# Performance work log

Hardware: AMD Instinct MI355X
Metric: run time of the kernel (lower is better)

Reference implementation:

```python
import jax, jax.numpy as jnp
import numpy as np

B, T, D = 2, 2048, 2048
N, K, H = 16, 8, 128  # num_heads, num_kv_heads, head_dim
SOFTCAP = 50.0
ROPE_BASE = 10000.0


def apply_rope(x, positions):
    # x: [B, L, heads, H], positions: [B, L]
    head_dim = x.shape[-1]
    fraction = 2.0 * jnp.arange(head_dim // 2, dtype=jnp.float32) / head_dim
    timescale = ROPE_BASE ** fraction  # [H/2]
    sinusoid = positions.astype(jnp.float32)[..., None] / timescale  # [B, L, H/2]
    sinusoid = sinusoid[..., None, :]  # [B, L, 1, H/2]
    sin, cos = jnp.sin(sinusoid), jnp.cos(sinusoid)
    first, second = jnp.split(x, 2, axis=-1)
    out = jnp.concatenate([first * cos - second * sin,
                           second * cos + first * sin], axis=-1)
    return out.astype(x.dtype)


def setup_inputs() -> dict:
    key = jax.random.key(0)
    kx, kq, kkv, ko = jax.random.split(key, 4)
    x = jax.random.normal(kx, (B, T, D), dtype=jnp.float32)
    positions = jnp.broadcast_to(jnp.arange(T, dtype=jnp.int32), (B, T))
    attn_mask = jnp.broadcast_to(
        jnp.tril(jnp.ones((T, T), dtype=bool))[None, None], (B, 1, T, T))
    # variance-scaling fan_in init approximated with scaled normals
    w_q = jax.random.normal(kq, (N, D, H), dtype=jnp.float32) / np.sqrt(D)
    w_kv = jax.random.normal(kkv, (2, K, D, H), dtype=jnp.float32) / np.sqrt(D)
    w_out = jax.random.normal(ko, (N, H, D), dtype=jnp.float32) / np.sqrt(N * H)
    return {"x": x, "positions": positions, "attn_mask": attn_mask,
            "w_q": w_q, "w_kv": w_kv, "w_out": w_out}


def reference(x, positions, attn_mask, w_q, w_kv, w_out):
    # QKV projections (GQA: separate q and kv einsums)
    q = jnp.einsum('BTD,NDH->BTNH', x, w_q)        # [B,T,N,H]
    kv = jnp.einsum('BSD,cKDH->cBSKH', x, w_kv)     # [2,B,S,K,H]
    k, v = kv[0], kv[1]
    q = apply_rope(q, positions) * (H ** -0.5)      # rsqrt_head_dim norm
    k = apply_rope(k, positions)
    # GQA grouping: N = K * G
    G = N // K
    qg = q.reshape(B, T, K, G, H)
    logits = jnp.einsum('BTKGH,BSKH->BKGTS', qg, k).astype(jnp.float32)
    logits = jnp.tanh(logits / SOFTCAP) * SOFTCAP   # logits softcap
    big_neg = -2.3819763e+38
    masked = jnp.where(attn_mask[:, :, None, :, :], logits, big_neg)
    probs = jax.nn.softmax(masked, axis=-1).astype(k.dtype)
    encoded = jnp.einsum('BKGTS,BSKH->BTKGH', probs, v).reshape(B, T, N, H)
    return jnp.einsum('BTNH,NHD->BTD', encoded, w_out)
```

## Files before the change

### kernel.cpp

```cpp
#include <hip/hip_runtime.h>
#include <math.h>
#include <stdint.h>


typedef unsigned short u16;
using bf16x8 = __attribute__((ext_vector_type(8))) short;
using f32x4  = __attribute__((ext_vector_type(4))) float;

#define MFMA_BF16(a,b,c) __builtin_amdgcn_mfma_f32_16x16x32_bf16((a),(b),(c),0,0,0)

static __device__ __forceinline__ float b2f(u16 u) {
  union { unsigned int i; float f; } v; v.i = ((unsigned int)u) << 16; return v.f;
}
static __device__ __forceinline__ u16 f2b(float f) {
  union { float f; unsigned int i; } v; v.f = f;
  unsigned int r = v.i + 0x7fffu + ((v.i >> 16) & 1u);
  return (u16)(r >> 16);
}
static __device__ __forceinline__ unsigned pk2(float x0, float x1) {
  union { float f; unsigned u; } a, b;
  a.f = x0; b.f = x1;
  return __builtin_amdgcn_perm(b.u + 0x8000u, a.u + 0x8000u, 0x07060302u);
}
static __device__ __forceinline__ void gload_lds16(const void* g, void* l) {
  __builtin_amdgcn_global_load_lds((__attribute__((address_space(1))) void*)(g),
                                   (__attribute__((address_space(3))) void*)(l),
                                   16, 0, 0);
}

__global__ __launch_bounds__(256) void prep(const float* __restrict__ x, u16* __restrict__ xb,
                                            const float* __restrict__ wq,
                                            const float* __restrict__ wkv,
                                            const float* __restrict__ wout,
                                            u16* __restrict__ wqkvt, u16* __restrict__ woutt) {
  const int tid = threadIdx.x;
  int bid = blockIdx.x;
  if (bid < 8192) {
    const int i = (bid * 256 + tid) * 4;
    const float4 v = *(const float4*)(x + i);
    ushort4 o;
    o.x = f2b(v.x); o.y = f2b(v.y); o.z = f2b(v.z); o.w = f2b(v.w);
    *(ushort4*)(xb + i) = o;
    return;
  }
  bid -= 8192;
  const float* src;
  u16* dst;
  int rows, cols, bx, by;
  if (bid < 8192) {
    const int seg = bid >> 12;
    const int r = bid & 4095;
    const int mat = r >> 8;
    bx = (r & 255) & 3;
    by = (r & 255) >> 2;
    rows = 2048; cols = 128;
    src = (seg ? wkv : wq) + (size_t)mat * 2048 * 128;
    dst = wqkvt + (size_t)(seg * 16 + mat) * 2048 * 128;
  } else {
    const int r = bid - 8192;
    bx = r & 63;
    by = r >> 6;
    rows = 2048; cols = 2048;
    src = wout;
    dst = woutt;
  }
  __shared__ u16 tile[32][33];
  const int c0 = bx * 32, r0 = by * 32;
  const int tx = tid & 31, ty = tid >> 5;
#pragma unroll
  for (int j = 0; j < 4; ++j)
    tile[ty + j * 8][tx] = f2b(src[(size_t)(r0 + ty + j * 8) * cols + (c0 + tx)]);
  __syncthreads();
#pragma unroll
  for (int j = 0; j < 4; ++j)
    dst[(size_t)(c0 + ty + j * 8) * rows + (r0 + tx)] = tile[tx][ty + j * 8];
}

__global__ __launch_bounds__(512, 2) void gemm_qkv(const u16* __restrict__ X,
                                                   const u16* __restrict__ wqkvt,
                                                   u16* __restrict__ qb,
                                                   u16* __restrict__ kb,
                                                   u16* __restrict__ vtb) {
  __shared__ __align__(16) u16 sAB[2][2][16384];
  const int m0 = blockIdx.x * 256;
  const int ct0 = blockIdx.y * 2;
  const u16* BT = wqkvt + (size_t)blockIdx.y * 256 * 2048;
  const int tid = threadIdx.x;
  const int wave = tid >> 6, lane = tid & 63;
  const int wm = wave >> 2, wn = wave & 3;
  const int quad = lane >> 4, l16 = lane & 15;
  const int srow = lane >> 3;
  const int sch = (lane & 7) ^ srow;

  f32x4 acc[8][4] = {};

  auto STAGE = [&](int kt, int bsel) {
    const int k0 = kt * 64;
#pragma unroll
    for (int s = 0; s < 4; ++s) {
      const int ia = wave * 4 + s;
      const int row = ia * 8 + srow;
      gload_lds16(X + (size_t)(m0 + row) * 2048 + k0 + sch * 8,
                  (char*)&sAB[bsel][0][0] + ia * 1024);
      gload_lds16(BT + (size_t)row * 2048 + k0 + sch * 8,
                  (char*)&sAB[bsel][1][0] + ia * 1024);
    }
  };

  auto COMPUTE = [&](int bsel) {
    const char* aB = (const char*)&sAB[bsel][0][0];
    const char* bB = (const char*)&sAB[bsel][1][0];
#pragma unroll
    for (int ks = 0; ks < 2; ++ks) {
      bf16x8 bfr[4];
#pragma unroll
      for (int nf = 0; nf < 4; ++nf) {
        const int Rb = wn * 64 + nf * 16 + l16;
        bfr[nf] = *(const bf16x8*)(bB + Rb * 128 + (((ks * 4 + quad) ^ (Rb & 7)) << 4));
      }
      __builtin_amdgcn_s_setprio(1);
#pragma unroll
      for (int mf = 0; mf < 8; ++mf) {
        const int R = wm * 128 + mf * 16 + l16;
        const bf16x8 af = *(const bf16x8*)(aB + R * 128 + (((ks * 4 + quad) ^ (R & 7)) << 4));
#pragma unroll
        for (int nf = 0; nf < 4; ++nf)
          acc[mf][nf] = MFMA_BF16(af, bfr[nf], acc[mf][nf]);
      }
      __builtin_amdgcn_s_setprio(0);
    }
  };

  STAGE(0, 0);
#pragma unroll 1
  for (int t = 0; t < 31; ++t) {
    STAGE(t + 1, (t + 1) & 1);
    asm volatile("s_waitcnt vmcnt(8)" ::: "memory");
    __builtin_amdgcn_s_barrier();
    asm volatile("" ::: "memory");
    COMPUTE(t & 1);
    asm volatile("" ::: "memory");
    __builtin_amdgcn_s_barrier();
    asm volatile("" ::: "memory");
  }
  asm volatile("s_waitcnt vmcnt(0)" ::: "memory");
  __builtin_amdgcn_s_barrier();
  asm volatile("" ::: "memory");
  COMPUTE(1);

#pragma unroll
  for (int mf = 0; mf < 8; ++mf) {
    const int mm = m0 + wm * 128 + mf * 16 + quad * 4;
    const int b = mm >> 11;
    const int t = mm & 2047;
#pragma unroll
    for (int nf = 0; nf < 4; ++nf) {
      const int colg = wn * 64 + nf * 16;
      const int ct = ct0 + (colg >> 7);
      const int h = (colg & 127) + l16;
      if (ct < 16) {
        u16* d = qb + (((size_t)b * 16 + ct) * 2048 + t) * 128 + h;
#pragma unroll
        for (int i = 0; i < 4; ++i) d[(size_t)i * 128] = f2b(acc[mf][nf][i]);
      } else if (ct < 24) {
        u16* d = kb + (((size_t)b * 8 + (ct - 16)) * 2048 + t) * 128 + h;
#pragma unroll
        for (int i = 0; i < 4; ++i) d[(size_t)i * 128] = f2b(acc[mf][nf][i]);
      } else {
        u16* d = vtb + (((size_t)b * 8 + (ct - 24)) * 128 + h) * 2048 + t;
        uint2 pkv;
        pkv.x = (unsigned)f2b(acc[mf][nf][0]) | ((unsigned)f2b(acc[mf][nf][1]) << 16);
        pkv.y = (unsigned)f2b(acc[mf][nf][2]) | ((unsigned)f2b(acc[mf][nf][3]) << 16);
        *(uint2*)d = pkv;
      }
    }
  }
}

__global__ __launch_bounds__(256) void rope_kernel(u16* __restrict__ qb,
                                                   u16* __restrict__ kb,
                                                   const int* __restrict__ pos) {
  const unsigned idx = blockIdx.x * 256 + threadIdx.x;
  const unsigned QP = 1u << 21;
  u16* p;
  float scale;
  int b, t, j2;
  if (idx < QP) {
    j2 = (int)(idx & 31) * 2; t = (int)((idx >> 5) & 2047);
    const int hd = (int)((idx >> 16) & 15); b = (int)(idx >> 20);
    p = qb + (((size_t)b * 16 + hd) * 2048 + t) * 128;
    scale = 0.08838834764831845f;
  } else {
    const unsigned r = idx - QP;
    j2 = (int)(r & 31) * 2; t = (int)((r >> 5) & 2047);
    const int hd = (int)((r >> 16) & 7); b = (int)(r >> 19);
    p = kb + (((size_t)b * 8 + hd) * 2048 + t) * 128;
    scale = 1.0f;
  }
  const float fpos = (float)pos[(size_t)b * 2048 + t];
  const unsigned lo = *(const unsigned*)(p + j2);
  const unsigned hi = *(const unsigned*)(p + j2 + 64);
  unsigned olo = 0, ohi = 0;
#pragma unroll
  for (int d = 0; d < 2; ++d) {
    const int j = j2 + d;
    const float ts = __powf(10000.0f, (float)j * (1.0f / 64.0f));
    float sn, cs;
    sincosf(fpos / ts, &sn, &cs);
    const float a = b2f((u16)((d ? (lo >> 16) : lo) & 0xffffu));
    const float c2 = b2f((u16)((d ? (hi >> 16) : hi) & 0xffffu));
    olo |= ((unsigned)f2b((a * cs - c2 * sn) * scale)) << (16 * d);
    ohi |= ((unsigned)f2b((c2 * cs + a * sn) * scale)) << (16 * d);
  }
  *(unsigned*)(p + j2) = olo;
  *(unsigned*)(p + j2 + 64) = ohi;
}

__global__ __launch_bounds__(256, 2) void attn_fused(const u16* __restrict__ qg,
                                                     const u16* __restrict__ kg,
                                                     const u16* __restrict__ vtg,
                                                     u16* __restrict__ enc) {
  __shared__ __align__(16) char lds[2][32768];

  const int bid = blockIdx.x;
  const int half = bid >> 9;
  const int r = bid & 511;
  const int x = r & 7;
  const int g = r >> 3;
  const int pr = g & 15;
  const int head = (g >> 4) * 8 + x;
  const int Q = half ? pr : (31 - pr);
  const int b = head >> 4;
  const int n = head & 15;
  const int kh = n >> 1;

  const u16* qbase = qg + ((size_t)b * 16 + n) * 2048 * 128;
  const u16* kbase = kg + ((size_t)b * 8 + kh) * 2048 * 128;
  const u16* vbase = vtg + ((size_t)b * 8 + kh) * 128 * 2048;

  const int tid = threadIdx.x, wave = tid >> 6, lane = tid & 63;
  const int quad = lane >> 4, l16 = lane & 15;
  const int bp_a0 = ((quad & 1) * 32 + l16) * 4;
  const int bp_a1 = bp_a0 + 64;

  const float L2E = 1.4426950408889634f;
  const float C50 = 72.13475204444817f;
  const float A1 = 1.3333333333e-4f;
  const float A2 = 2.1333333333e-8f;
  const float A3 = 3.4539682540e-12f;

  const u16* kp[4];
  const u16* vp[4];
#pragma unroll
  for (int s = 0; s < 4; ++s) {
    const int kr = wave * 16 + s * 4 + quad;
    kp[s] = kbase + (size_t)kr * 128 + (l16 ^ (s * 4 + quad)) * 8;
    const int vr = wave * 32 + s * 8 + (lane >> 3);
    vp[s] = vbase + (size_t)vr * 2048 + ((lane & 7) ^ (lane >> 3)) * 8;
  }

  auto STAGE = [&](int bsel) {
    char* base = &lds[bsel][0];
#pragma unroll
    for (int s = 0; s < 4; ++s) {
      gload_lds16(kp[s], base + (wave * 4 + s) * 1024);
      gload_lds16(vp[s], base + 16384 + (wave * 4 + s) * 1024);
      kp[s] += 64 * 128;
      vp[s] += 64;
    }
  };

  const int tw = Q * 64 + wave * 16;
  const int tlane = tw + l16;

  bf16x8 qf[4];
#pragma unroll
  for (int kf = 0; kf < 4; ++kf)
    qf[kf] = *(const bf16x8*)(qbase + (size_t)tlane * 128 + kf * 32 + quad * 8);

  f32x4 o[8] = {};
  f32x4 lacc = {0.f, 0.f, 0.f, 0.f};

  STAGE(0);

#pragma unroll 1
  for (int si = 0; si <= Q; ++si) {
    const int s0 = si * 64;
    if (si < Q) {
      STAGE((si + 1) & 1);
      asm volatile("s_waitcnt vmcnt(8)" ::: "memory");
    } else {
      asm volatile("s_waitcnt vmcnt(0)" ::: "memory");
    }
    __builtin_amdgcn_s_barrier();
    asm volatile("" ::: "memory");

    const char* sK = &lds[si & 1][0];
    const char* sV = &lds[si & 1][0] + 16384;

    const bool diag = (si == Q);
    const int nfmax = diag ? wave : 3;
    const int kmax = diag ? (wave >> 1) : 1;

    f32x4 sacc[4];
#pragma unroll
    for (int nf = 0; nf < 4; ++nf) {
      if (nf <= nfmax) {
        const int sr = nf * 16 + l16;
        f32x4 a = {0.f, 0.f, 0.f, 0.f};
#pragma unroll
        for (int kf = 0; kf < 4; ++kf) {
          const bf16x8 kfr =
              *(const bf16x8*)(sK + sr * 256 + (((kf * 4 + quad) ^ (sr & 15)) << 4));
          a = MFMA_BF16(kfr, qf[kf], a);
        }
        sacc[nf] = a;
      }
    }

#pragma unroll
    for (int nf = 0; nf < 4; ++nf) {
      if (nf <= nfmax) {
        const f32x4 xv = sacc[nf];
        const f32x4 u = xv * xv;
        f32x4 t = u * (-A3) + A2;
        t = u * t + (-A1);
        t = u * t + 1.0f;
        const f32x4 tc = xv * t;
        f32x4 pv;
#pragma unroll
        for (int i = 0; i < 4; ++i) pv[i] = exp2f(fmaf(tc[i], L2E, -C50));
        if (diag) {
#pragma unroll
          for (int i = 0; i < 4; ++i) {
            const int sg = s0 + nf * 16 + quad * 4 + i;
            if (sg > tlane) pv[i] = 0.0f;
          }
        }
        sacc[nf] = pv;
        lacc += pv;
      }
    }

    unsigned pkd[4][2];
#pragma unroll
    for (int nf = 0; nf < 4; ++nf) {
      if (nf <= nfmax) {
        pkd[nf][0] = pk2(sacc[nf][0], sacc[nf][1]);
        pkd[nf][1] = pk2(sacc[nf][2], sacc[nf][3]);
      } else {
        pkd[nf][0] = 0u; pkd[nf][1] = 0u;
      }
    }

#pragma unroll
    for (int c2 = 0; c2 < 2; ++c2) {
      if (c2 <= kmax) {
        const int lo = (quad >> 1);
        const int dA0 = __builtin_amdgcn_ds_bpermute(bp_a0, (int)pkd[2 * c2][0]);
        const int dB0 = __builtin_amdgcn_ds_bpermute(bp_a0, (int)pkd[2 * c2 + 1][0]);
        const int dA1 = __builtin_amdgcn_ds_bpermute(bp_a0, (int)pkd[2 * c2][1]);
        const int dB1 = __builtin_amdgcn_ds_bpermute(bp_a0, (int)pkd[2 * c2 + 1][1]);
        const int dA2 = __builtin_amdgcn_ds_bpermute(bp_a1, (int)pkd[2 * c2][0]);
        const int dB2 = __builtin_amdgcn_ds_bpermute(bp_a1, (int)pkd[2 * c2 + 1][0]);
        const int dA3 = __builtin_amdgcn_ds_bpermute(bp_a1, (int)pkd[2 * c2][1]);
        const int dB3 = __builtin_amdgcn_ds_bpermute(bp_a1, (int)pkd[2 * c2 + 1][1]);
        union { int d[4]; bf16x8 v; } pb;
        pb.d[0] = lo ? dB0 : dA0;
        pb.d[1] = lo ? dB1 : dA1;
        pb.d[2] = lo ? dB2 : dA2;
        pb.d[3] = lo ? dB3 : dA3;
#pragma unroll
        for (int nfo = 0; nfo < 8; ++nfo) {
          const int hr = nfo * 16 + l16;
          const bf16x8 vb =
              *(const bf16x8*)(sV + hr * 128 + (((c2 * 4 + quad) ^ (hr & 7)) << 4));
          o[nfo] = MFMA_BF16(vb, pb.v, o[nfo]);
        }
      }
    }
    asm volatile("" ::: "memory");
    __builtin_amdgcn_s_barrier();
    asm volatile("" ::: "memory");
  }

  float lsum = lacc[0] + lacc[1] + lacc[2] + lacc[3];
  lsum += __shfl_xor(lsum, 16);
  lsum += __shfl_xor(lsum, 32);
  const float inv = 1.0f / lsum;
  u16* d = enc + (((size_t)b * 2048 + tlane) * 16 + n) * 128 + quad * 4;
#pragma unroll
  for (int nfo = 0; nfo < 8; ++nfo) {
    uint2 st;
    st.x = (unsigned)f2b(o[nfo][0] * inv) | ((unsigned)f2b(o[nfo][1] * inv) << 16);
    st.y = (unsigned)f2b(o[nfo][2] * inv) | ((unsigned)f2b(o[nfo][3] * inv) << 16);
    *(uint2*)(d + nfo * 16) = st;
  }
}

__global__ __launch_bounds__(512, 2) void gemm_out(const u16* __restrict__ A,
                                                   const u16* __restrict__ Bt,
                                                   float* __restrict__ C) {
  __shared__ __align__(16) u16 sA[2][16384];
  __shared__ __align__(16) u16 sB[2][8192];
  const int m0 = blockIdx.x * 256;
  const int n0 = blockIdx.y * 128;
  const int tid = threadIdx.x;
  const int wave = tid >> 6, lane = tid & 63;
  const int wm = wave >> 2, wn = wave & 3;
  const int quad = lane >> 4, l16 = lane & 15;
  const int srow = lane >> 3;
  const int sch = (lane & 7) ^ srow;

  f32x4 acc[8][2] = {};

  auto STAGE = [&](int kt, int bsel) {
    const int k0 = kt * 64;
#pragma unroll
    for (int s = 0; s < 4; ++s) {
      const int ia = wave * 4 + s;
      const int row = ia * 8 + srow;
      gload_lds16(A + (size_t)(m0 + row) * 2048 + k0 + sch * 8,
                  (char*)&sA[bsel][0] + ia * 1024);
    }
#pragma unroll
    for (int s = 0; s < 2; ++s) {
      const int ib = wave * 2 + s;
      const int row = ib * 8 + srow;
      gload_lds16(Bt + (size_t)(n0 + row) * 2048 + k0 + sch * 8,
                  (char*)&sB[bsel][0] + ib * 1024);
    }
  };

  auto COMPUTE = [&](int bsel) {
    const char* aB = (const char*)&sA[bsel][0];
    const char* bB = (const char*)&sB[bsel][0];
#pragma unroll
    for (int ks = 0; ks < 2; ++ks) {
      bf16x8 bfr[2];
#pragma unroll
      for (int nf = 0; nf < 2; ++nf) {
        const int Rb = wn * 32 + nf * 16 + l16;
        bfr[nf] = *(const bf16x8*)(bB + Rb * 128 + (((ks * 4 + quad) ^ (Rb & 7)) << 4));
      }
      __builtin_amdgcn_s_setprio(1);
#pragma unroll
      for (int mf = 0; mf < 8; ++mf) {
        const int R = wm * 128 + mf * 16 + l16;
        const bf16x8 af = *(const bf16x8*)(aB + R * 128 + (((ks * 4 + quad) ^ (R & 7)) << 4));
#pragma unroll
        for (int nf = 0; nf < 2; ++nf)
          acc[mf][nf] = MFMA_BF16(af, bfr[nf], acc[mf][nf]);
      }
      __builtin_amdgcn_s_setprio(0);
    }
  };

  STAGE(0, 0);
#pragma unroll 1
  for (int t = 0; t < 31; ++t) {
    STAGE(t + 1, (t + 1) & 1);
    asm volatile("s_waitcnt vmcnt(6)" ::: "memory");
    __builtin_amdgcn_s_barrier();
    asm volatile("" ::: "memory");
    COMPUTE(t & 1);
    asm volatile("" ::: "memory");
    __builtin_amdgcn_s_barrier();
    asm volatile("" ::: "memory");
  }
  asm volatile("s_waitcnt vmcnt(0)" ::: "memory");
  __builtin_amdgcn_s_barrier();
  asm volatile("" ::: "memory");
  COMPUTE(1);

#pragma unroll
  for (int mf = 0; mf < 8; ++mf) {
    const int mm = m0 + wm * 128 + mf * 16 + quad * 4;
#pragma unroll
    for (int nf = 0; nf < 2; ++nf) {
      const int col = n0 + wn * 32 + nf * 16 + l16;
#pragma unroll
      for (int i = 0; i < 4; ++i) C[(size_t)(mm + i) * 2048 + col] = acc[mf][nf][i];
    }
  }
}

extern "C" void kernel_launch(void* const* d_in, const int* in_sizes, int n_in,
                              void* d_out, int out_size, void* d_ws, size_t ws_size,
                              hipStream_t stream) {
  (void)in_sizes; (void)n_in; (void)out_size; (void)ws_size;
  const float* x     = (const float*)d_in[0];
  const int*   posi  = (const int*)d_in[1];
  const float* w_q   = (const float*)d_in[3];
  const float* w_kv  = (const float*)d_in[4];
  const float* w_out = (const float*)d_in[5];
  float* out = (float*)d_out;

  u16* ws = (u16*)d_ws;
  u16* wqkvt = ws;
  u16* woutt = ws + (size_t)8388608;
  u16* qb    = ws + (size_t)12582912;
  u16* kb    = ws + (size_t)20971520;
  u16* vtb   = ws + (size_t)25165824;
  u16* encb  = ws + (size_t)29360128;
  u16* xb    = encb;

  prep<<<20480, 256, 0, stream>>>(x, xb, w_q, w_kv, w_out, wqkvt, woutt);
  gemm_qkv<<<dim3(16, 16), 512, 0, stream>>>(xb, wqkvt, qb, kb, vtb);
  rope_kernel<<<12288, 256, 0, stream>>>(qb, kb, posi);
  attn_fused<<<1024, 256, 0, stream>>>(qb, kb, vtb, encb);
  gemm_out<<<dim3(16, 16), 512, 0, stream>>>(encb, woutt, out);
}
```

Baseline: 386.3 us.

## Single-buffer attention LDS, raise occupancy to 4 blocks, fold log2e into softcap polynomial

Replaces the double-buffered K/V LDS staging with one 32KB buffer that is loaded synchronously each iteration between two barriers, and raises launch bounds to 4 blocks per CU. The goal is more resident waves, so latency is hidden by occupancy instead of software prefetch. The softcap tanh polynomial now has log2(e) folded into its coefficients, which removes a multiply, and the exp is done with a raw v_exp_f32 instead of exp2f, which drops range handling. The trade-off is that global-to-LDS loads no longer overlap compute within a block, and there is register pressure at the higher occupancy bound.

```diff
diff --git a/kernel.cpp b/kernel.cpp
--- a/kernel.cpp
+++ b/kernel.cpp
@@ -21,6 +21,11 @@
   union { float f; unsigned u; } a, b;
   a.f = x0; b.f = x1;
   return __builtin_amdgcn_perm(b.u + 0x8000u, a.u + 0x8000u, 0x07060302u);
+}
+static __device__ __forceinline__ float rexp2(float a) {
+  float r;
+  asm("v_exp_f32 %0, %1" : "=v"(r) : "v"(a));
+  return r;
 }
 static __device__ __forceinline__ void gload_lds16(const void* g, void* l) {
   __builtin_amdgcn_global_load_lds((__attribute__((address_space(1))) void*)(g),
@@ -216,11 +221,13 @@
   *(unsigned*)(p + j2 + 64) = ohi;
 }
 
-__global__ __launch_bounds__(256, 2) void attn_fused(const u16* __restrict__ qg,
+__global__ __launch_bounds__(256, 4) void attn_fused(const u16* __restrict__ qg,
                                                      const u16* __restrict__ kg,
                                                      const u16* __restrict__ vtg,
                                                      u16* __restrict__ enc) {
-  __shared__ __align__(16) char lds[2][32768];
+  __shared__ __align__(16) char lds[32768];
+  char* sK = lds;
+  char* sV = lds + 16384;
 
   const int bid = blockIdx.x;
   const int half = bid >> 9;
@@ -245,9 +252,9 @@
 
   const float L2E = 1.4426950408889634f;
   const float C50 = 72.13475204444817f;
-  const float A1 = 1.3333333333e-4f;
-  const float A2 = 2.1333333333e-8f;
-  const float A3 = 3.4539682540e-12f;
+  const float B1 = 1.9235933879e-4f;
+  const float B2 = 3.0777494206e-8f;
+  const float B3 = 4.9830224200e-12f;
 
   const u16* kp[4];
   const u16* vp[4];
@@ -259,17 +266,6 @@
     vp[s] = vbase + (size_t)vr * 2048 + ((lane & 7) ^ (lane >> 3)) * 8;
   }
 
-  auto STAGE = [&](int bsel) {
-    char* base = &lds[bsel][0];
-#pragma unroll
-    for (int s = 0; s < 4; ++s) {
-      gload_lds16(kp[s], base + (wave * 4 + s) * 1024);
-      gload_lds16(vp[s], base + 16384 + (wave * 4 + s) * 1024);
-      kp[s] += 64 * 128;
-      vp[s] += 64;
-    }
-  };
-
   const int tw = Q * 64 + wave * 16;
   const int tlane = tw + l16;
 
@@ -280,23 +276,19 @@
 
   f32x4 o[8] = {};
   f32x4 lacc = {0.f, 0.f, 0.f, 0.f};
-
-  STAGE(0);
 
 #pragma unroll 1
   for (int si = 0; si <= Q; ++si) {
     const int s0 = si * 64;
-    if (si < Q) {
-      STAGE((si + 1) & 1);
-      asm volatile("s_waitcnt vmcnt(8)" ::: "memory");
-    } else {
-      asm volatile("s_waitcnt vmcnt(0)" ::: "memory");
-    }
-    __builtin_amdgcn_s_barrier();
-    asm volatile("" ::: "memory");
-
-    const char* sK = &lds[si & 1][0];
-    const char* sV = &lds[si & 1][0] + 16384;
+    __syncthreads();
+#pragma unroll
+    for (int s = 0; s < 4; ++s) {
+      gload_lds16(kp[s], sK + (wave * 4 + s) * 1024);
+      gload_lds16(vp[s], sV + (wave * 4 + s) * 1024);
+      kp[s] += 64 * 128;
+      vp[s] += 64;
+    }
+    __syncthreads();
 
     const bool diag = (si == Q);
     const int nfmax = diag ? wave : 3;
@@ -323,13 +315,12 @@
       if (nf <= nfmax) {
         const f32x4 xv = sacc[nf];
         const f32x4 u = xv * xv;
-        f32x4 t = u * (-A3) + A2;
-        t = u * t + (-A1);
-        t = u * t + 1.0f;
-        const f32x4 tc = xv * t;
+        f32x4 t = u * (-B3) + B2;
+        t = u * t + (-B1);
+        t = u * t + L2E;
         f32x4 pv;
 #pragma unroll
-        for (int i = 0; i < 4; ++i) pv[i] = exp2f(fmaf(tc[i], L2E, -C50));
+        for (int i = 0; i < 4; ++i) pv[i] = rexp2(fmaf(xv[i], t[i], -C50));
         if (diag) {
 #pragma unroll
           for (int i = 0; i < 4; ++i) {
@@ -379,9 +370,6 @@
         }
       }
     }
-    asm volatile("" ::: "memory");
-    __builtin_amdgcn_s_barrier();
-    asm volatile("" ::: "memory");
   }
 
   float lsum = lacc[0] + lacc[1] + lacc[2] + lacc[3];
```

New measurement: 358.0 us. -7.3%, faster.
